# Kernel tuning notes

Measured on AMD Instinct MI355X. Metric: run time of the kernel, lower is better.

## Reference

```python
import jax, jax.numpy as jnp
import numpy as np
import math

PRE_D = 2048   # pre_d_model (scaled from 8192)
D = 4096       # d_model (scaled from 16384)
N = 64         # d_state (scaled from 128)
K = 4          # d_conv
EXP = 2
L = 128        # sequence_length
DI1 = EXP * PRE_D
DI2 = EXP * D
DTR1 = math.ceil(PRE_D / 16)
DTR2 = math.ceil(D / 16)


def _sinusoid(max_len, d):
    pe = np.zeros((max_len, d), np.float32)
    pos = np.arange(max_len, dtype=np.float32)[:, None]
    div = np.exp(np.arange(0, d, 2, dtype=np.float32) * (-math.log(10000.0) / d))
    pe[:, 0::2] = np.sin(pos * div)
    pe[:, 1::2] = np.cos(pos * div)
    return jnp.asarray(pe)


def _mamba_params(key, d_in, d_out, di, dtr, n, k):
    ks = jax.random.split(key, 6)
    s = 0.02
    dt = jnp.exp(jax.random.uniform(ks[4], (di,)) * (math.log(0.1) - math.log(1e-3)) + math.log(1e-3))
    return dict(
        in_proj=jax.random.normal(ks[0], (2 * di, d_in)) * s,
        conv_w=jax.random.normal(ks[1], (di, k)) * s,
        conv_b=jnp.zeros((di,)),
        x_proj=jax.random.normal(ks[2], (dtr + 2 * n, di)) * s,
        dt_w=jax.random.normal(ks[3], (di, dtr)) * s,
        dt_b=jnp.log(jnp.expm1(dt)),  # softplus^-1 of dt init
        A_log=jnp.log(jnp.tile(jnp.arange(1, n + 1, dtype=jnp.float32), (di, 1))),
        D=jnp.ones((di,)),
        out_proj=jax.random.normal(ks[5], (d_out, di)) * s,
    )


def setup_inputs() -> dict:
    key = jax.random.key(0)
    k1, k2, k3, k4 = jax.random.split(key, 4)
    inp = {
        'pe': _sinusoid(L, PRE_D),                              # (L, PRE_D)
        'to_cond_w': jax.random.normal(k3, (PRE_D, 1)) * 0.02,  # Linear(1 -> PRE_D)
        'to_cond_b': jnp.zeros((PRE_D,)),
        'condition': jax.random.normal(k4, (1,)),
        'batch': 1,
    }
    for pref, p in (('m1_', _mamba_params(k1, PRE_D, PRE_D, DI1, DTR1, N, K)),
                    ('m2_', _mamba_params(k2, PRE_D, D, DI2, DTR2, N, K))):
        for name, v in p.items():
            inp[pref + name] = v
    return inp


def _silu(x):
    return x * jax.nn.sigmoid(x)


def _mamba(x, in_w, cw, cb, xp_w, dt_w, dt_b, A_log, Dp, out_w, dtr, n):
    # x: (B, L, d_in)
    xz = x @ in_w.T                     # (B, L, 2*di)
    xr, z = jnp.split(xz, 2, axis=-1)
    kk = cw.shape[1]
    Lx = xr.shape[1]
    xpad = jnp.pad(xr, ((0, 0), (kk - 1, 0), (0, 0)))  # causal pad
    conv = sum(cw[:, i] * xpad[:, i:i + Lx, :] for i in range(kk)) + cb
    xr = _silu(conv)
    dbc = xr @ xp_w.T                   # (B, L, dtr + 2n)
    dt = dbc[..., :dtr]
    Bm = dbc[..., dtr:dtr + n]
    Cm = dbc[..., dtr + n:]
    dt = jax.nn.softplus(dt @ dt_w.T + dt_b)           # (B, L, di)
    A = -jnp.exp(A_log)                                 # (di, n)
    dA = jnp.exp(jnp.einsum('bld,dn->bldn', dt, A))
    dBx = jnp.einsum('bld,bln,bld->bldn', dt, Bm, xr)

    def comb(c1, c2):
        a1, b1 = c1
        a2, b2 = c2
        return a2 * a1, a2 * b1 + b2

    _, h = jax.lax.associative_scan(comb, (dA, dBx), axis=1)  # (B, L, di, n)
    y = jnp.einsum('bldn,bln->bld', h, Cm) + xr * Dp
    y = y * _silu(z)
    return y @ out_w.T


def reference(pe, to_cond_w, to_cond_b, condition,
              m1_in_proj, m1_conv_w, m1_conv_b, m1_x_proj, m1_dt_w, m1_dt_b, m1_A_log, m1_D, m1_out_proj,
              m2_in_proj, m2_conv_w, m2_conv_b, m2_x_proj, m2_dt_w, m2_dt_b, m2_A_log, m2_D, m2_out_proj,
              batch):
    cond = condition.reshape(-1, 1, 1)
    c = jnp.einsum('bli,oi->blo', cond, to_cond_w) + to_cond_b   # (Bc,1,PRE_D)
    x = jnp.tile(pe[None], (batch, 1, 1)) + c                    # (B, L, PRE_D)
    x = _mamba(x, m1_in_proj, m1_conv_w, m1_conv_b, m1_x_proj, m1_dt_w, m1_dt_b,
               m1_A_log, m1_D, m1_out_proj, DTR1, N)
    x = _mamba(x, m2_in_proj, m2_conv_w, m2_conv_b, m2_x_proj, m2_dt_w, m2_dt_b,
               m2_A_log, m2_D, m2_out_proj, DTR2, N)
    return x
```

## Files before the change

kernel.cpp:

```cpp
#include <hip/hip_runtime.h>
#include <hip/hip_bf16.h>
#include <math.h>


typedef __attribute__((ext_vector_type(8))) short short8_t;
typedef __attribute__((ext_vector_type(4))) float f32x4;

__device__ __forceinline__ float sigmoidf_(float x) {
  return 1.0f / (1.0f + __expf(-x));
}
__device__ __forceinline__ float softplusf_(float x) {
  return fmaxf(x, 0.0f) + log1pf(expf(-fabsf(x)));
}
__device__ __forceinline__ void splitbf(float f, ushort& h, ushort& lo) {
  __hip_bfloat16 hb = __float2bfloat16(f);
  h = *reinterpret_cast<ushort*>(&hb);
  float hf = __bfloat162float(hb);
  __hip_bfloat16 lb = __float2bfloat16(f - hf);
  lo = *reinterpret_cast<ushort*>(&lb);
}
__device__ __forceinline__ size_t poff(int l, int d) {
  return (size_t)(d >> 5) * 8192 + (size_t)((d >> 3) & 3) * 1024 +
         (size_t)l * 8 + (d & 7);
}

__global__ __launch_bounds__(256) void k_prep(const float* __restrict__ pe,
                                              const float* __restrict__ cw,
                                              const float* __restrict__ cb,
                                              const float* __restrict__ cond,
                                              ushort* __restrict__ xp) {
  int i = blockIdx.x * 256 + threadIdx.x;
  int d = i & 2047;
  int l = i >> 11;
  float v = pe[i] + cond[0] * cw[d] + cb[d];
  ushort h, lo;
  splitbf(v, h, lo);
  size_t o = poff(l, d);
  xp[o] = h;
  xp[o + 4096] = lo;
}

#define KSTEP 32
__global__ __launch_bounds__(256, 2) void k_gemm(const ushort* __restrict__ Ap,
                                                 const float* __restrict__ W, int ldw,
                                                 float* __restrict__ P,
                                                 int N, int Ks) {
  __shared__ ushort Ws[2][2][4][128][8];

  const int n0   = blockIdx.x * 128;
  const int s    = blockIdx.z;
  const int kbeg = s * Ks;
  const int t    = threadIdx.x;
  const int l    = t & 63;
  const int w    = t >> 6;
  const int wm   = w >> 1;
  const int wn   = w & 1;
  const int lr   = l & 15;
  const int lg   = l >> 4;

  f32x4 acc[4][4];
#pragma unroll
  for (int mi = 0; mi < 4; ++mi)
#pragma unroll
    for (int ni = 0; ni < 4; ++ni) acc[mi][ni] = (f32x4)(0.0f);

  const int srow = t >> 3;
  const int sk16 = t & 7;
  const int skb  = sk16 >> 1;
  const int se0  = (sk16 & 1) * 4;
  const float* pWg = W + (size_t)(n0 + srow) * ldw + kbeg + sk16 * 4;

  const ushort* pAc = Ap + (size_t)(kbeg >> 5) * 8192;
  const int arow = 64 * wm + lr;
  const int brow = 64 * wn + lr;

  const int nIter = Ks / KSTEP;
  float4 wv[4];

#pragma unroll
  for (int r = 0; r < 4; ++r)
    wv[r] = *(const float4*)(pWg + (size_t)(r * 32) * ldw);
#pragma unroll
  for (int r = 0; r < 4; ++r) {
    ushort4 h4, l4;
    splitbf(wv[r].x, h4.x, l4.x); splitbf(wv[r].y, h4.y, l4.y);
    splitbf(wv[r].z, h4.z, l4.z); splitbf(wv[r].w, h4.w, l4.w);
    *(ushort4*)&Ws[0][0][skb][srow + 32 * r][se0] = h4;
    *(ushort4*)&Ws[0][1][skb][srow + 32 * r][se0] = l4;
  }
  __syncthreads();

  for (int j = 0; j < nIter; ++j) {
    const int bi = j & 1;
    const bool more = (j + 1 < nIter);

    const ushort* pAj = pAc + (size_t)j * 8192;
    short8_t ah[4], al[4];
#pragma unroll
    for (int mi = 0; mi < 4; ++mi) {
      const size_t fo = (size_t)lg * 1024 + (size_t)(arow + 16 * mi) * 8;
      ah[mi] = *(const short8_t*)(pAj + fo);
      al[mi] = *(const short8_t*)(pAj + 4096 + fo);
    }
    if (more) {
      const size_t ko = (size_t)(j + 1) * KSTEP;
#pragma unroll
      for (int r = 0; r < 4; ++r)
        wv[r] = *(const float4*)(pWg + ko + (size_t)(r * 32) * ldw);
    }
    short8_t bh[4], bl[4];
#pragma unroll
    for (int ni = 0; ni < 4; ++ni) {
      bh[ni] = *(const short8_t*)&Ws[bi][0][lg][brow + 16 * ni][0];
      bl[ni] = *(const short8_t*)&Ws[bi][1][lg][brow + 16 * ni][0];
    }
#pragma unroll
    for (int mi = 0; mi < 4; ++mi)
#pragma unroll
      for (int ni = 0; ni < 4; ++ni) {
        acc[mi][ni] = __builtin_amdgcn_mfma_f32_16x16x32_bf16(ah[mi], bh[ni], acc[mi][ni], 0, 0, 0);
        acc[mi][ni] = __builtin_amdgcn_mfma_f32_16x16x32_bf16(al[mi], bh[ni], acc[mi][ni], 0, 0, 0);
        acc[mi][ni] = __builtin_amdgcn_mfma_f32_16x16x32_bf16(ah[mi], bl[ni], acc[mi][ni], 0, 0, 0);
      }
    if (more) {
#pragma unroll
      for (int r = 0; r < 4; ++r) {
        ushort4 h4, l4;
        splitbf(wv[r].x, h4.x, l4.x); splitbf(wv[r].y, h4.y, l4.y);
        splitbf(wv[r].z, h4.z, l4.z); splitbf(wv[r].w, h4.w, l4.w);
        *(ushort4*)&Ws[bi ^ 1][0][skb][srow + 32 * r][se0] = h4;
        *(ushort4*)&Ws[bi ^ 1][1][skb][srow + 32 * r][se0] = l4;
      }
    }
    __syncthreads();
  }

  float* Pd = P + (size_t)s * 128 * N + n0 + 64 * wn;
#pragma unroll
  for (int mi = 0; mi < 4; ++mi)
#pragma unroll
    for (int ni = 0; ni < 4; ++ni) {
#pragma unroll
      for (int jj = 0; jj < 4; ++jj) {
        const int m = 64 * wm + 16 * mi + 4 * lg + jj;
        Pd[(size_t)m * N + 16 * ni + lr] = acc[mi][ni][jj];
      }
    }
}

__global__ __launch_bounds__(256) void k_reduce(const float* __restrict__ P,
                                                float* __restrict__ Y,
                                                ushort* __restrict__ Yp,
                                                int MN, int N, int S, int ep,
                                                const float* __restrict__ bias) {
  int i = (blockIdx.x * 256 + threadIdx.x) * 4;
  if (i >= MN) return;
  float4 v = *(const float4*)&P[i];
  for (int s = 1; s < S; ++s) {
    float4 p = *(const float4*)&P[(size_t)s * MN + i];
    v.x += p.x; v.y += p.y; v.z += p.z; v.w += p.w;
  }
  int n = i % N;
  int l = i / N;
  if (ep & 1) {
    const float4 b = *(const float4*)&bias[n];
    v.x = softplusf_(v.x + b.x);
    v.y = softplusf_(v.y + b.y);
    v.z = softplusf_(v.z + b.z);
    v.w = softplusf_(v.w + b.w);
  }
  if (ep & 4) *(float4*)&Y[i] = v;
  if (ep & 2) {
    ushort4 h4, l4;
    splitbf(v.x, h4.x, l4.x);
    splitbf(v.y, h4.y, l4.y);
    splitbf(v.z, h4.z, l4.z);
    splitbf(v.w, h4.w, l4.w);
    size_t o = poff(l, n);
    *(ushort4*)&Yp[o] = h4;
    *(ushort4*)&Yp[o + 4096] = l4;
  }
}

__global__ __launch_bounds__(256) void k_reduceA(const float* __restrict__ P,
                                                 float* __restrict__ Y, int MN) {
  int g = blockIdx.y;
  int i = (blockIdx.x * 256 + threadIdx.x) * 4;
  if (i >= MN) return;
  const float* Pp = P + (size_t)g * 8 * MN;
  float4 v = *(const float4*)&Pp[i];
  for (int s = 1; s < 8; ++s) {
    float4 p = *(const float4*)&Pp[(size_t)s * MN + i];
    v.x += p.x; v.y += p.y; v.z += p.z; v.w += p.w;
  }
  *(float4*)&Y[(size_t)g * MN + i] = v;
}

__global__ __launch_bounds__(256) void k_conv_silu(const float* __restrict__ xz,
                                                   const float* __restrict__ cw,
                                                   const float* __restrict__ cb,
                                                   float* __restrict__ xc,
                                                   ushort* __restrict__ xcp,
                                                   int DI, int lg2DI) {
  int i = blockIdx.x * 256 + threadIdx.x;
  int l = i >> lg2DI;
  int d = i & (DI - 1);
  const float4 w = *(const float4*)&cw[d * 4];
  const float* xr = xz + d;
  int ld = 2 * DI;
  float s = cb[d];
  s += w.w * xr[l * ld];
  if (l >= 1) s += w.z * xr[(l - 1) * ld];
  if (l >= 2) s += w.y * xr[(l - 2) * ld];
  if (l >= 3) s += w.x * xr[(l - 3) * ld];
  float v = s * sigmoidf_(s);
  xc[i] = v;
  ushort h, lo;
  splitbf(v, h, lo);
  size_t o = poff(l, d);
  xcp[o] = h;
  xcp[o + 4096] = lo;
}

__global__ __launch_bounds__(256) void k_scan(const float* __restrict__ dt,
                                              const float* __restrict__ xc,
                                              const float* __restrict__ dbc,
                                              const float* __restrict__ A_log,
                                              const float* __restrict__ Dp,
                                              float* __restrict__ y,
                                              int DI, int DTR) {
  __shared__ float cs[4][32][65];
  const int wid = threadIdx.x >> 6;
  const int n   = threadIdx.x & 63;
  const int d   = blockIdx.x * 4 + wid;
  const int du  = __builtin_amdgcn_readfirstlane(d);
  const float A  = -__expf(A_log[(size_t)du * 64 + n]);
  const float Dd = Dp[du];
  const int ldbc = DTR + 128;
  const float* Bp = dbc + DTR + n;
  const float* Cp = dbc + DTR + 64 + n;
  float h = 0.0f;
  for (int l0 = 0; l0 < 128; l0 += 32) {
#pragma unroll 8
    for (int l = l0; l < l0 + 32; ++l) {
      float dtv = dt[(size_t)l * DI + du];
      float xcv = xc[(size_t)l * DI + du];
      float dA  = __expf(dtv * A);
      float bx  = dtv * xcv;
      h = fmaf(dA, h, bx * Bp[(size_t)l * ldbc]);
      cs[wid][l - l0][n] = h * Cp[(size_t)l * ldbc];
    }
    __syncthreads();
    const int r = n & 31, hf = n >> 5;
    float ssum = 0.0f;
#pragma unroll
    for (int j = 0; j < 32; ++j) ssum += cs[wid][r][hf * 32 + j];
    ssum += __shfl_xor(ssum, 32, 64);
    if (n < 32) {
      int ll = l0 + r;
      float xcv = xc[(size_t)ll * DI + du];
      y[(size_t)ll * DI + du] = ssum + xcv * Dd;
    }
    __syncthreads();
  }
}

__global__ __launch_bounds__(256) void k_gate(const float* __restrict__ yb,
                                              const float* __restrict__ xz,
                                              ushort* __restrict__ yp,
                                              int DI, int lg2DI) {
  int i = blockIdx.x * 256 + threadIdx.x;
  int l = i >> lg2DI;
  int d = i & (DI - 1);
  float z = xz[((size_t)l << (lg2DI + 1)) + DI + d];
  float v = yb[i] * (z * sigmoidf_(z));
  ushort h, lo;
  splitbf(v, h, lo);
  size_t o = poff(l, d);
  yp[o] = h;
  yp[o + 4096] = lo;
}

struct GemmCtx {
  float* part;
  float* part2;
  long long cap;
};

static inline void gemm(const ushort* Ap, const float* W, int ldw,
                        float* dstF, ushort* dstP,
                        int N, int K, int Sdes, int ep,
                        const float* bias, const GemmCtx& cx, hipStream_t stream) {
  int S = Sdes;
  if (S > K / KSTEP) S = K / KSTEP;
  if (S < 1) S = 1;
  while (S > 1 && (long long)S * 128 * N > cx.cap) S >>= 1;
  const int Ks = K / S;
  const bool direct = (S == 1 && ep == 4);
  dim3 g(N / 128, 1, S);
  float* dst = direct ? dstF : cx.part;
  k_gemm<<<g, 256, 0, stream>>>(Ap, W, ldw, dst, N, Ks);
  if (direct) return;
  const int MN = 128 * N;
  const int rb = (MN / 4 + 255) / 256;
  if (S <= 16) {
    k_reduce<<<rb, 256, 0, stream>>>(cx.part, dstF, dstP, MN, N, S, ep, bias);
  } else {
    k_reduceA<<<dim3(rb, S / 8), 256, 0, stream>>>(cx.part, cx.part2, MN);
    k_reduce<<<rb, 256, 0, stream>>>(cx.part2, dstF, dstP, MN, N, S / 8, ep, bias);
  }
}

extern "C" void kernel_launch(void* const* d_in, const int* in_sizes, int n_in,
                              void* d_out, int out_size, void* d_ws, size_t ws_size,
                              hipStream_t stream) {
  const float* pe        = (const float*)d_in[0];
  const float* to_cond_w = (const float*)d_in[1];
  const float* to_cond_b = (const float*)d_in[2];
  const float* condition = (const float*)d_in[3];
  const int o = (in_sizes[4] == 1) ? 5 : 4;
  const float* m1_in_proj  = (const float*)d_in[o + 0];
  const float* m1_conv_w   = (const float*)d_in[o + 1];
  const float* m1_conv_b   = (const float*)d_in[o + 2];
  const float* m1_x_proj   = (const float*)d_in[o + 3];
  const float* m1_dt_w     = (const float*)d_in[o + 4];
  const float* m1_dt_b     = (const float*)d_in[o + 5];
  const float* m1_A_log    = (const float*)d_in[o + 6];
  const float* m1_D        = (const float*)d_in[o + 7];
  const float* m1_out_proj = (const float*)d_in[o + 8];
  const float* m2_in_proj  = (const float*)d_in[o + 9];
  const float* m2_conv_w   = (const float*)d_in[o + 10];
  const float* m2_conv_b   = (const float*)d_in[o + 11];
  const float* m2_x_proj   = (const float*)d_in[o + 12];
  const float* m2_dt_w     = (const float*)d_in[o + 13];
  const float* m2_dt_b     = (const float*)d_in[o + 14];
  const float* m2_A_log    = (const float*)d_in[o + 15];
  const float* m2_D        = (const float*)d_in[o + 16];
  const float* m2_out_proj = (const float*)d_in[o + 17];

  float* ws = (float*)d_ws;
  float*  xz   = ws;
  float*  xc   = ws + 2097152;
  float*  dbc  = ws + 3145728;
  float*  dtb  = ws + 3194880;
  float*  yb   = ws + 4243456;
  ushort* x0p  = (ushort*)(ws + 5292032);
  ushort* xcp  = (ushort*)(ws + 5554176);
  ushort* dbcp = (ushort*)(ws + 6602752);
  ushort* ybp  = (ushort*)(ws + 6651904);
  ushort* midp = (ushort*)(ws + 7700480);
  float*  part2 = ws + 7962624;
  float*  part  = ws + 8749056;

  GemmCtx cx;
  cx.part = part;
  cx.part2 = part2;
  cx.cap = (long long)(ws_size / 4) - 8749056;
  if (cx.cap < 0) cx.cap = 0;

  k_prep<<<1024, 256, 0, stream>>>(pe, to_cond_w, to_cond_b, condition, x0p);

  gemm(x0p, m1_in_proj, 2048, xz, nullptr, 8192, 2048, 4, 4, nullptr, cx, stream);
  k_conv_silu<<<(128 * 4096) / 256, 256, 0, stream>>>(xz, m1_conv_w, m1_conv_b,
                                                      xc, xcp, 4096, 12);
  gemm(xcp, m1_x_proj, 4096, dbc, dbcp, 256, 4096, 128, 6, nullptr, cx, stream);
  gemm(dbcp, m1_dt_w, 128, dtb, nullptr, 4096, 128, 4, 5, m1_dt_b, cx, stream);
  k_scan<<<1024, 256, 0, stream>>>(dtb, xc, dbc, m1_A_log, m1_D, yb, 4096, 128);
  k_gate<<<(128 * 4096) / 256, 256, 0, stream>>>(yb, xz, ybp, 4096, 12);
  gemm(ybp, m1_out_proj, 4096, nullptr, midp, 2048, 4096, 16, 2, nullptr, cx, stream);

  gemm(midp, m2_in_proj, 2048, xz, nullptr, 16384, 2048, 2, 4, nullptr, cx, stream);
  k_conv_silu<<<(128 * 8192) / 256, 256, 0, stream>>>(xz, m2_conv_w, m2_conv_b,
                                                      xc, xcp, 8192, 13);
  gemm(xcp, m2_x_proj, 8192, dbc, dbcp, 384, 8192, 128, 6, nullptr, cx, stream);
  gemm(dbcp, m2_dt_w, 256, dtb, nullptr, 8192, 256, 4, 5, m2_dt_b, cx, stream);
  k_scan<<<2048, 256, 0, stream>>>(dtb, xc, dbc, m2_A_log, m2_D, yb, 8192, 256);
  k_gate<<<(128 * 8192) / 256, 256, 0, stream>>>(yb, xz, ybp, 8192, 13);
  gemm(ybp, m2_out_proj, 8192, (float*)d_out, nullptr, 4096, 8192, 8, 4, nullptr, cx, stream);
}
```

Measured before the change: 398.1 us.

## Add wide-K 64-column GEMM kernel with double-buffered weight tiles for large projections

Adds a new GEMM kernel that processes 128-wide K chunks per iteration over 64-column output tiles, double-buffers the split-bf16 weight tile in shared memory, and prefetches the next chunk's weights into registers while the MFMAs run. Blocks start at staggered K offsets so concurrent blocks spread their weight reads. It is used for the in_proj and out_proj GEMMs, which dominate weight traffic, while the small x_proj and dt GEMMs keep the old kernel. The aim is fewer barriers per unit of K and more blocks in flight for the weight-streaming projections. The cost is higher register pressure from holding 32 A fragments and 16 prefetched weight pairs per thread.

Result: faster. 378.2 us (-5.0%).

```diff
diff --git a/kernel.cpp b/kernel.cpp
--- a/kernel.cpp
+++ b/kernel.cpp
@@ -38,6 +38,121 @@
   size_t o = poff(l, d);
   xp[o] = h;
   xp[o + 4096] = lo;
+}
+
+#define KW 128
+__global__ __launch_bounds__(256, 2) void k_gemmW(const ushort* __restrict__ Ap,
+                                                  const float* __restrict__ W, int ldw,
+                                                  float* __restrict__ P,
+                                                  int N, int Ks) {
+  __shared__ ushort Ws[2][2][16][66][8];
+
+  const int n0   = blockIdx.x * 64;
+  const int s    = blockIdx.z;
+  const int kbeg = s * Ks;
+  const int t    = threadIdx.x;
+  const int l    = t & 63;
+  const int w    = t >> 6;
+  const int wm   = w >> 1;
+  const int wn   = w & 1;
+  const int lr   = l & 15;
+  const int lg   = l >> 4;
+
+  f32x4 acc[4][2];
+#pragma unroll
+  for (int mi = 0; mi < 4; ++mi)
+#pragma unroll
+    for (int ni = 0; ni < 2; ++ni) acc[mi][ni] = (f32x4)(0.0f);
+
+  const int nIter = Ks / KW;
+  const int j0    = (blockIdx.x * 3 + s) & (nIter - 1);
+
+  const float* pWg = W + (size_t)(n0 + 16 * w) * ldw + kbeg + 2 * l;
+  const int skb = l >> 2;
+  const int se  = 2 * (l & 3);
+  const ushort* pA0 = Ap + (size_t)(kbeg >> 5) * 8192;
+  const int arow = 64 * wm + lr;
+  const int brow = 32 * wn + lr;
+
+#pragma unroll
+  for (int i = 0; i < 16; ++i) {
+    float2 v = *(const float2*)(pWg + (size_t)i * ldw + (size_t)j0 * KW);
+    ushort h0, lo0, h1, lo1;
+    splitbf(v.x, h0, lo0);
+    splitbf(v.y, h1, lo1);
+    ushort2 hh; hh.x = h0; hh.y = h1;
+    ushort2 ll; ll.x = lo0; ll.y = lo1;
+    *(ushort2*)&Ws[0][0][skb][16 * w + i][se] = hh;
+    *(ushort2*)&Ws[0][1][skb][16 * w + i][se] = ll;
+  }
+  __syncthreads();
+
+  for (int jj = 0; jj < nIter; ++jj) {
+    const int cur = (j0 + jj) & (nIter - 1);
+    const int bi  = jj & 1;
+    const bool more = (jj + 1 < nIter);
+
+    short8_t ah[4][4], al[4][4];
+#pragma unroll
+    for (int c = 0; c < 4; ++c) {
+      const ushort* pAj = pA0 + (size_t)(cur * 4 + c) * 8192;
+#pragma unroll
+      for (int mi = 0; mi < 4; ++mi) {
+        const size_t fo = (size_t)lg * 1024 + (size_t)(arow + 16 * mi) * 8;
+        ah[c][mi] = *(const short8_t*)(pAj + fo);
+        al[c][mi] = *(const short8_t*)(pAj + 4096 + fo);
+      }
+    }
+    float2 wv[16];
+    if (more) {
+      const size_t ko = (size_t)((j0 + jj + 1) & (nIter - 1)) * KW;
+#pragma unroll
+      for (int i = 0; i < 16; ++i)
+        wv[i] = *(const float2*)(pWg + (size_t)i * ldw + ko);
+    }
+#pragma unroll
+    for (int c = 0; c < 4; ++c) {
+      short8_t bh[2], bl[2];
+#pragma unroll
+      for (int ni = 0; ni < 2; ++ni) {
+        bh[ni] = *(const short8_t*)&Ws[bi][0][c * 4 + lg][brow + 16 * ni][0];
+        bl[ni] = *(const short8_t*)&Ws[bi][1][c * 4 + lg][brow + 16 * ni][0];
+      }
+#pragma unroll
+      for (int mi = 0; mi < 4; ++mi)
+#pragma unroll
+        for (int ni = 0; ni < 2; ++ni) {
+          acc[mi][ni] = __builtin_amdgcn_mfma_f32_16x16x32_bf16(ah[c][mi], bh[ni], acc[mi][ni], 0, 0, 0);
+          acc[mi][ni] = __builtin_amdgcn_mfma_f32_16x16x32_bf16(al[c][mi], bh[ni], acc[mi][ni], 0, 0, 0);
+          acc[mi][ni] = __builtin_amdgcn_mfma_f32_16x16x32_bf16(ah[c][mi], bl[ni], acc[mi][ni], 0, 0, 0);
+        }
+    }
+    if (more) {
+#pragma unroll
+      for (int i = 0; i < 16; ++i) {
+        ushort h0, lo0, h1, lo1;
+        splitbf(wv[i].x, h0, lo0);
+        splitbf(wv[i].y, h1, lo1);
+        ushort2 hh; hh.x = h0; hh.y = h1;
+        ushort2 ll; ll.x = lo0; ll.y = lo1;
+        *(ushort2*)&Ws[bi ^ 1][0][skb][16 * w + i][se] = hh;
+        *(ushort2*)&Ws[bi ^ 1][1][skb][16 * w + i][se] = ll;
+      }
+    }
+    __syncthreads();
+  }
+
+  float* Pd = P + (size_t)s * 128 * N + n0 + 32 * wn;
+#pragma unroll
+  for (int mi = 0; mi < 4; ++mi)
+#pragma unroll
+    for (int ni = 0; ni < 2; ++ni) {
+#pragma unroll
+      for (int jj = 0; jj < 4; ++jj) {
+        const int m = 64 * wm + 16 * mi + 4 * lg + jj;
+        Pd[(size_t)m * N + 16 * ni + lr] = acc[mi][ni][jj];
+      }
+    }
 }
 
 #define KSTEP 32
@@ -287,10 +402,23 @@
   long long cap;
 };
 
-static inline void gemm(const ushort* Ap, const float* W, int ldw,
-                        float* dstF, ushort* dstP,
-                        int N, int K, int Sdes, int ep,
-                        const float* bias, const GemmCtx& cx, hipStream_t stream) {
+static inline void reduce_stage(float* dstF, ushort* dstP, int N, int S, int ep,
+                                const float* bias, const GemmCtx& cx,
+                                hipStream_t stream) {
+  const int MN = 128 * N;
+  const int rb = (MN / 4 + 255) / 256;
+  if (S <= 16) {
+    k_reduce<<<rb, 256, 0, stream>>>(cx.part, dstF, dstP, MN, N, S, ep, bias);
+  } else {
+    k_reduceA<<<dim3(rb, S / 8), 256, 0, stream>>>(cx.part, cx.part2, MN);
+    k_reduce<<<rb, 256, 0, stream>>>(cx.part2, dstF, dstP, MN, N, S / 8, ep, bias);
+  }
+}
+
+static inline void gemmS(const ushort* Ap, const float* W, int ldw,
+                         float* dstF, ushort* dstP,
+                         int N, int K, int Sdes, int ep,
+                         const float* bias, const GemmCtx& cx, hipStream_t stream) {
   int S = Sdes;
   if (S > K / KSTEP) S = K / KSTEP;
   if (S < 1) S = 1;
@@ -298,17 +426,23 @@
   const int Ks = K / S;
   const bool direct = (S == 1 && ep == 4);
   dim3 g(N / 128, 1, S);
-  float* dst = direct ? dstF : cx.part;
-  k_gemm<<<g, 256, 0, stream>>>(Ap, W, ldw, dst, N, Ks);
-  if (direct) return;
-  const int MN = 128 * N;
-  const int rb = (MN / 4 + 255) / 256;
-  if (S <= 16) {
-    k_reduce<<<rb, 256, 0, stream>>>(cx.part, dstF, dstP, MN, N, S, ep, bias);
-  } else {
-    k_reduceA<<<dim3(rb, S / 8), 256, 0, stream>>>(cx.part, cx.part2, MN);
-    k_reduce<<<rb, 256, 0, stream>>>(cx.part2, dstF, dstP, MN, N, S / 8, ep, bias);
-  }
+  k_gemm<<<g, 256, 0, stream>>>(Ap, W, ldw, direct ? dstF : cx.part, N, Ks);
+  if (!direct) reduce_stage(dstF, dstP, N, S, ep, bias, cx, stream);
+}
+
+static inline void gemmW(const ushort* Ap, const float* W, int ldw,
+                         float* dstF, ushort* dstP,
+                         int N, int K, int Sdes, int ep,
+                         const float* bias, const GemmCtx& cx, hipStream_t stream) {
+  int S = Sdes;
+  if (S > K / KW) S = K / KW;
+  if (S < 1) S = 1;
+  while (S > 1 && (long long)S * 128 * N > cx.cap) S >>= 1;
+  const int Ks = K / S;
+  const bool direct = (S == 1 && ep == 4);
+  dim3 g(N / 64, 1, S);
+  k_gemmW<<<g, 256, 0, stream>>>(Ap, W, ldw, direct ? dstF : cx.part, N, Ks);
+  if (!direct) reduce_stage(dstF, dstP, N, S, ep, bias, cx, stream);
 }
 
 extern "C" void kernel_launch(void* const* d_in, const int* in_sizes, int n_in,
@@ -360,21 +494,21 @@
 
   k_prep<<<1024, 256, 0, stream>>>(pe, to_cond_w, to_cond_b, condition, x0p);
 
-  gemm(x0p, m1_in_proj, 2048, xz, nullptr, 8192, 2048, 4, 4, nullptr, cx, stream);
+  gemmW(x0p, m1_in_proj, 2048, xz, nullptr, 8192, 2048, 4, 4, nullptr, cx, stream);
   k_conv_silu<<<(128 * 4096) / 256, 256, 0, stream>>>(xz, m1_conv_w, m1_conv_b,
                                                       xc, xcp, 4096, 12);
-  gemm(xcp, m1_x_proj, 4096, dbc, dbcp, 256, 4096, 128, 6, nullptr, cx, stream);
-  gemm(dbcp, m1_dt_w, 128, dtb, nullptr, 4096, 128, 4, 5, m1_dt_b, cx, stream);
+  gemmS(xcp, m1_x_proj, 4096, dbc, dbcp, 256, 4096, 128, 6, nullptr, cx, stream);
+  gemmS(dbcp, m1_dt_w, 128, dtb, nullptr, 4096, 128, 4, 5, m1_dt_b, cx, stream);
   k_scan<<<1024, 256, 0, stream>>>(dtb, xc, dbc, m1_A_log, m1_D, yb, 4096, 128);
   k_gate<<<(128 * 4096) / 256, 256, 0, stream>>>(yb, xz, ybp, 4096, 12);
-  gemm(ybp, m1_out_proj, 4096, nullptr, midp, 2048, 4096, 16, 2, nullptr, cx, stream);
-
-  gemm(midp, m2_in_proj, 2048, xz, nullptr, 16384, 2048, 2, 4, nullptr, cx, stream);
+  gemmW(ybp, m1_out_proj, 4096, nullptr, midp, 2048, 4096, 16, 2, nullptr, cx, stream);
+
+  gemmW(midp, m2_in_proj, 2048, xz, nullptr, 16384, 2048, 2, 4, nullptr, cx, stream);
   k_conv_silu<<<(128 * 8192) / 256, 256, 0, stream>>>(xz, m2_conv_w, m2_conv_b,
                                                       xc, xcp, 8192, 13);
-  gemm(xcp, m2_x_proj, 8192, dbc, dbcp, 384, 8192, 128, 6, nullptr, cx, stream);
-  gemm(dbcp, m2_dt_w, 256, dtb, nullptr, 8192, 256, 4, 5, m2_dt_b, cx, stream);
+  gemmS(xcp, m2_x_proj, 8192, dbc, dbcp, 384, 8192, 128, 6, nullptr, cx, stream);
+  gemmS(dbcp, m2_dt_w, 256, dtb, nullptr, 8192, 256, 4, 5, m2_dt_b, cx, stream);
   k_scan<<<2048, 256, 0, stream>>>(dtb, xc, dbc, m2_A_log, m2_D, yb, 8192, 256);
   k_gate<<<(128 * 8192) / 256, 256, 0, stream>>>(yb, xz, ybp, 8192, 13);
-  gemm(ybp, m2_out_proj, 8192, (float*)d_out, nullptr, 4096, 8192, 8, 4, nullptr, cx, stream);
-}
+  gemmW(ybp, m2_out_proj, 8192, (float*)d_out, nullptr, 4096, 8192, 8, 4, nullptr, cx, stream);
+}
```

## Add narrow-N weight-streaming GEMM with LDS async loads for large projections

Applied to the files above, without the earlier changes.

Adds a new GEMM kernel that gives each block 16 output columns and the full K range, so no split-K partial buffers or reduction kernels are needed. It streams the fp32 weight rows into double-buffered LDS through global_load_lds, with an XOR swizzle and staggered start chunks across blocks. Weights are split into bf16 hi/lo by truncation rather than rounding. The in_proj and out_proj GEMMs now use this kernel, which removes the reduction passes and extra partial-buffer traffic on the bandwidth-bound weight reads. The cost is fewer MFMA ops per weight element and reliance on the A operand being re-read from cache by every block.

Result: slower. 429.4 us (+7.9%).

```diff
diff --git a/kernel.cpp b/kernel.cpp
--- a/kernel.cpp
+++ b/kernel.cpp
@@ -19,9 +19,20 @@
   __hip_bfloat16 lb = __float2bfloat16(f - hf);
   lo = *reinterpret_cast<ushort*>(&lb);
 }
+__device__ __forceinline__ void tsplit(float f, ushort& h, ushort& lo) {
+  unsigned u = __float_as_uint(f);
+  h = (ushort)(u >> 16);
+  float r = f - __uint_as_float(u & 0xFFFF0000u);
+  lo = (ushort)(__float_as_uint(r) >> 16);
+}
 __device__ __forceinline__ size_t poff(int l, int d) {
   return (size_t)(d >> 5) * 8192 + (size_t)((d >> 3) & 3) * 1024 +
          (size_t)l * 8 + (d & 7);
+}
+__device__ __forceinline__ void g2l16(const float* g, float* lp) {
+  __builtin_amdgcn_global_load_lds(
+      (const __attribute__((address_space(1))) unsigned int*)g,
+      (__attribute__((address_space(3))) unsigned int*)lp, 16, 0, 0);
 }
 
 __global__ __launch_bounds__(256) void k_prep(const float* __restrict__ pe,
@@ -38,6 +49,113 @@
   size_t o = poff(l, d);
   xp[o] = h;
   xp[o + 4096] = lo;
+}
+
+#define KC 256
+__global__ __launch_bounds__(256, 2) void k_gemmWL(const ushort* __restrict__ Ap,
+                                                   const float* __restrict__ W, int ldw,
+                                                   float* __restrict__ dstF,
+                                                   ushort* __restrict__ dstP,
+                                                   int N, int K, int ep) {
+  __shared__ float Wl[2][16][KC];
+
+  const int n0 = blockIdx.x * 16;
+  const int t  = threadIdx.x;
+  const int l  = t & 63;
+  const int w  = t >> 6;
+  const int lr = l & 15;
+  const int lg = l >> 4;
+
+  f32x4 acc[2];
+  acc[0] = (f32x4)(0.0f);
+  acc[1] = (f32x4)(0.0f);
+
+  const int nSC = K / KC;
+  const int j0  = blockIdx.x % nSC;
+
+  const float* gsrc[4];
+  float* gdst[4];
+#pragma unroll
+  for (int q = 0; q < 4; ++q) {
+    const int r = 4 * w + q;
+    gsrc[q] = W + (size_t)(n0 + r) * ldw + (size_t)(l ^ (r & 7)) * 4;
+    gdst[q] = &Wl[0][r][0];
+  }
+  const int ldsStride = 16 * KC;
+
+  size_t aoff[2];
+#pragma unroll
+  for (int mi = 0; mi < 2; ++mi)
+    aoff[mi] = (size_t)lg * 1024 + (size_t)(32 * w + 16 * mi + lr) * 8;
+
+#pragma unroll
+  for (int q = 0; q < 4; ++q)
+    g2l16(gsrc[q] + (size_t)j0 * KC, gdst[q]);
+  __syncthreads();
+
+  for (int j = 0; j < nSC; ++j) {
+    const int bi = j & 1;
+    const int sc = (j0 + j) % nSC;
+
+    short8_t ah[8][2], al[8][2];
+#pragma unroll
+    for (int ks = 0; ks < 8; ++ks) {
+      const ushort* pAc = Ap + (size_t)(sc * 8 + ks) * 8192;
+#pragma unroll
+      for (int mi = 0; mi < 2; ++mi) {
+        ah[ks][mi] = *(const short8_t*)(pAc + aoff[mi]);
+        al[ks][mi] = *(const short8_t*)(pAc + 4096 + aoff[mi]);
+      }
+    }
+    __builtin_amdgcn_sched_barrier(0);
+    if (j + 1 < nSC) {
+      const int scn = (j0 + j + 1) % nSC;
+#pragma unroll
+      for (int q = 0; q < 4; ++q)
+        g2l16(gsrc[q] + (size_t)scn * KC, gdst[q] + (bi ^ 1) * ldsStride);
+    }
+#pragma unroll
+    for (int ks = 0; ks < 8; ++ks) {
+      const int g0 = (ks * 8 + lg * 2) ^ (lr & 7);
+      const float4 vA = *(const float4*)&Wl[bi][lr][g0 * 4];
+      const float4 vB = *(const float4*)&Wl[bi][lr][(g0 ^ 1) * 4];
+      short8_t bh, bl;
+      {
+        const float f8[8] = {vA.x, vA.y, vA.z, vA.w, vB.x, vB.y, vB.z, vB.w};
+#pragma unroll
+        for (int e = 0; e < 8; ++e) {
+          ushort h, lo;
+          tsplit(f8[e], h, lo);
+          bh[e] = (short)h;
+          bl[e] = (short)lo;
+        }
+      }
+#pragma unroll
+      for (int mi = 0; mi < 2; ++mi) {
+        acc[mi] = __builtin_amdgcn_mfma_f32_16x16x32_bf16(ah[ks][mi], bh, acc[mi], 0, 0, 0);
+        acc[mi] = __builtin_amdgcn_mfma_f32_16x16x32_bf16(al[ks][mi], bh, acc[mi], 0, 0, 0);
+        acc[mi] = __builtin_amdgcn_mfma_f32_16x16x32_bf16(ah[ks][mi], bl, acc[mi], 0, 0, 0);
+      }
+    }
+    __syncthreads();
+  }
+
+#pragma unroll
+  for (int mi = 0; mi < 2; ++mi)
+#pragma unroll
+    for (int jj = 0; jj < 4; ++jj) {
+      const int m = 32 * w + 16 * mi + 4 * lg + jj;
+      const int n = n0 + lr;
+      const float v = acc[mi][jj];
+      if (ep & 4) dstF[(size_t)m * N + n] = v;
+      if (ep & 2) {
+        ushort h, lo;
+        splitbf(v, h, lo);
+        size_t o = poff(m, n);
+        dstP[o] = h;
+        dstP[o + 4096] = lo;
+      }
+    }
 }
 
 #define KSTEP 32
@@ -287,10 +405,23 @@
   long long cap;
 };
 
-static inline void gemm(const ushort* Ap, const float* W, int ldw,
-                        float* dstF, ushort* dstP,
-                        int N, int K, int Sdes, int ep,
-                        const float* bias, const GemmCtx& cx, hipStream_t stream) {
+static inline void reduce_stage(float* dstF, ushort* dstP, int N, int S, int ep,
+                                const float* bias, const GemmCtx& cx,
+                                hipStream_t stream) {
+  const int MN = 128 * N;
+  const int rb = (MN / 4 + 255) / 256;
+  if (S <= 16) {
+    k_reduce<<<rb, 256, 0, stream>>>(cx.part, dstF, dstP, MN, N, S, ep, bias);
+  } else {
+    k_reduceA<<<dim3(rb, S / 8), 256, 0, stream>>>(cx.part, cx.part2, MN);
+    k_reduce<<<rb, 256, 0, stream>>>(cx.part2, dstF, dstP, MN, N, S / 8, ep, bias);
+  }
+}
+
+static inline void gemmS(const ushort* Ap, const float* W, int ldw,
+                         float* dstF, ushort* dstP,
+                         int N, int K, int Sdes, int ep,
+                         const float* bias, const GemmCtx& cx, hipStream_t stream) {
   int S = Sdes;
   if (S > K / KSTEP) S = K / KSTEP;
   if (S < 1) S = 1;
@@ -298,17 +429,14 @@
   const int Ks = K / S;
   const bool direct = (S == 1 && ep == 4);
   dim3 g(N / 128, 1, S);
-  float* dst = direct ? dstF : cx.part;
-  k_gemm<<<g, 256, 0, stream>>>(Ap, W, ldw, dst, N, Ks);
-  if (direct) return;
-  const int MN = 128 * N;
-  const int rb = (MN / 4 + 255) / 256;
-  if (S <= 16) {
-    k_reduce<<<rb, 256, 0, stream>>>(cx.part, dstF, dstP, MN, N, S, ep, bias);
-  } else {
-    k_reduceA<<<dim3(rb, S / 8), 256, 0, stream>>>(cx.part, cx.part2, MN);
-    k_reduce<<<rb, 256, 0, stream>>>(cx.part2, dstF, dstP, MN, N, S / 8, ep, bias);
-  }
+  k_gemm<<<g, 256, 0, stream>>>(Ap, W, ldw, direct ? dstF : cx.part, N, Ks);
+  if (!direct) reduce_stage(dstF, dstP, N, S, ep, bias, cx, stream);
+}
+
+static inline void gemmWL(const ushort* Ap, const float* W, int K,
+                          float* dstF, ushort* dstP, int N, int ep,
+                          hipStream_t stream) {
+  k_gemmWL<<<dim3(N / 16), 256, 0, stream>>>(Ap, W, K, dstF, dstP, N, K, ep);
 }
 
 extern "C" void kernel_launch(void* const* d_in, const int* in_sizes, int n_in,
@@ -360,21 +488,21 @@
 
   k_prep<<<1024, 256, 0, stream>>>(pe, to_cond_w, to_cond_b, condition, x0p);
 
-  gemm(x0p, m1_in_proj, 2048, xz, nullptr, 8192, 2048, 4, 4, nullptr, cx, stream);
+  gemmWL(x0p, m1_in_proj, 2048, xz, nullptr, 8192, 4, stream);
   k_conv_silu<<<(128 * 4096) / 256, 256, 0, stream>>>(xz, m1_conv_w, m1_conv_b,
                                                       xc, xcp, 4096, 12);
-  gemm(xcp, m1_x_proj, 4096, dbc, dbcp, 256, 4096, 128, 6, nullptr, cx, stream);
-  gemm(dbcp, m1_dt_w, 128, dtb, nullptr, 4096, 128, 4, 5, m1_dt_b, cx, stream);
+  gemmS(xcp, m1_x_proj, 4096, dbc, dbcp, 256, 4096, 128, 6, nullptr, cx, stream);
+  gemmS(dbcp, m1_dt_w, 128, dtb, nullptr, 4096, 128, 4, 5, m1_dt_b, cx, stream);
   k_scan<<<1024, 256, 0, stream>>>(dtb, xc, dbc, m1_A_log, m1_D, yb, 4096, 128);
   k_gate<<<(128 * 4096) / 256, 256, 0, stream>>>(yb, xz, ybp, 4096, 12);
-  gemm(ybp, m1_out_proj, 4096, nullptr, midp, 2048, 4096, 16, 2, nullptr, cx, stream);
-
-  gemm(midp, m2_in_proj, 2048, xz, nullptr, 16384, 2048, 2, 4, nullptr, cx, stream);
+  gemmWL(ybp, m1_out_proj, 4096, nullptr, midp, 2048, 2, stream);
+
+  gemmWL(midp, m2_in_proj, 2048, xz, nullptr, 16384, 4, stream);
   k_conv_silu<<<(128 * 8192) / 256, 256, 0, stream>>>(xz, m2_conv_w, m2_conv_b,
                                                       xc, xcp, 8192, 13);
-  gemm(xcp, m2_x_proj, 8192, dbc, dbcp, 384, 8192, 128, 6, nullptr, cx, stream);
-  gemm(dbcp, m2_dt_w, 256, dtb, nullptr, 8192, 256, 4, 5, m2_dt_b, cx, stream);
+  gemmS(xcp, m2_x_proj, 8192, dbc, dbcp, 384, 8192, 128, 6, nullptr, cx, stream);
+  gemmS(dbcp, m2_dt_w, 256, dtb, nullptr, 8192, 256, 4, 5, m2_dt_b, cx, stream);
   k_scan<<<2048, 256, 0, stream>>>(dtb, xc, dbc, m2_A_log, m2_D, yb, 8192, 256);
   k_gate<<<(128 * 8192) / 256, 256, 0, stream>>>(yb, xz, ybp, 8192, 13);
-  gemm(ybp, m2_out_proj, 8192, (float*)d_out, nullptr, 4096, 8192, 8, 4, nullptr, cx, stream);
-}
+  gemmWL(ybp, m2_out_proj, 8192, (float*)d_out, nullptr, 4096, 4, stream);
+}
```
